# Kernel optimization log

Measured on AMD Instinct MI355X. Metric: run time of the kernel, lower is better.

Reference implementation:

```python
import jax, jax.numpy as jnp
import numpy as np

N, E, F, H, D, O = 100000, 1600000, 128, 128, 64, 1


def setup_inputs() -> dict:
    key = jax.random.key(0)
    ks = jax.random.split(key, 10)
    s = lambda f: np.float32(1.0 / np.sqrt(f))
    return {
        "x": jax.random.normal(ks[0], (N, F), jnp.float32),
        "edge_index": jax.random.randint(ks[1], (2, E), 0, N),
        "W1": jax.random.normal(ks[2], (F, H), jnp.float32) * s(F),
        "b1": jnp.zeros((H,), jnp.float32),
        "Wh": jax.random.normal(ks[3], (H, H), jnp.float32) * s(H),
        "bh": jnp.zeros((H,), jnp.float32),
        "W2": jax.random.normal(ks[4], (H, D), jnp.float32) * s(H),
        "b2": jnp.zeros((D,), jnp.float32),
        "Wo": jax.random.normal(ks[5], (D, O), jnp.float32) * s(D),
        "bo": jnp.zeros((O,), jnp.float32),
    }


def _gcn_layer(h, W, b, src, dst, norm, n):
    # linear transform then normalized sparse aggregation (GCNConv)
    h = h @ W                                   # [n, out]
    msg = h[src] * norm[:, None]                # gather + scale, [E+n, out]
    return jax.ops.segment_sum(msg, dst, num_segments=n) + b


def reference(x, edge_index, W1, b1, Wh, bh, W2, b2, Wo, bo):
    n = x.shape[0]
    loop = jnp.arange(n, dtype=edge_index.dtype)
    src = jnp.concatenate([edge_index[0], loop])  # add self loops
    dst = jnp.concatenate([edge_index[1], loop])
    deg = jax.ops.segment_sum(jnp.ones_like(dst, dtype=x.dtype), dst, num_segments=n)
    dinv = jnp.where(deg > 0, jax.lax.rsqrt(deg), 0.0)
    norm = dinv[src] * dinv[dst]                  # sym-normalized edge weights

    h = jax.nn.relu(_gcn_layer(x, W1, b1, src, dst, norm, n))
    h = jax.nn.relu(_gcn_layer(h, Wh, bh, src, dst, norm, n))
    z = _gcn_layer(h, W2, b2, src, dst, norm, n)  # embedding (no relu after gcn2)
    return z @ Wo + bo                            # node_classification logits [n, 1]
```

## Files before the change

kernel.cpp:

```cpp
#include <hip/hip_runtime.h>
#include <hip/hip_fp16.h>


#define CHUNK 8192
#define ASTR 136

using f16x8 = __attribute__((ext_vector_type(8))) _Float16;
using f32x4 = __attribute__((ext_vector_type(4))) float;

__global__ __launch_bounds__(256) void histH(const int* __restrict__ dst, int* __restrict__ hist,
                                             int E, int NBKT, int NB) {
    __shared__ int bins[1024];
    int blk = blockIdx.x;
    for (int i = threadIdx.x; i < NBKT; i += 256) bins[i] = 0;
    __syncthreads();
    int beg = blk * CHUNK, end = min(E, beg + CHUNK);
    for (int e = beg + threadIdx.x; e < end; e += 256)
        atomicAdd(&bins[dst[e] >> 7], 1);
    __syncthreads();
    for (int i = threadIdx.x; i < NBKT; i += 256)
        hist[i * NB + blk] = bins[i];
}

__global__ __launch_bounds__(256) void scanA(int* __restrict__ hist, int* __restrict__ binsum,
                                             int NBKT, int NB) {
    int wave = (int)((blockIdx.x * (size_t)blockDim.x + threadIdx.x) >> 6);
    if (wave >= NBKT) return;
    int lane = threadIdx.x & 63;
    int* row = hist + (size_t)wave * NB;
    int running = 0;
    for (int b0 = 0; b0 < NB; b0 += 64) {
        int idx = b0 + lane;
        int v = (idx < NB) ? row[idx] : 0;
        int s = v;
#pragma unroll
        for (int off = 1; off < 64; off <<= 1) {
            int u = __shfl_up(s, off, 64);
            if (lane >= off) s += u;
        }
        if (idx < NB) row[idx] = running + s - v;
        running += __shfl(s, 63, 64);
    }
    if (lane == 0) binsum[wave] = running;
}

__global__ void scanK2(const int* __restrict__ binsum, int* __restrict__ binbase,
                       int NBKT, int E) {
    __shared__ int s[1024];
    int t = threadIdx.x;
    int v = (t < NBKT) ? binsum[t] : 0;
    s[t] = v;
    __syncthreads();
    for (int off = 1; off < 1024; off <<= 1) {
        int u = (t >= off) ? s[t - off] : 0;
        __syncthreads();
        s[t] += u;
        __syncthreads();
    }
    if (t < NBKT) binbase[t] = s[t] - v;
    if (t == 0) binbase[NBKT] = E;
}

__global__ __launch_bounds__(256) void scatterH(const int* __restrict__ src,
                                                const int* __restrict__ dst,
                                                const int* __restrict__ hist,
                                                const int* __restrict__ binbase,
                                                int* __restrict__ tmp,
                                                int E, int NBKT, int NB) {
    __shared__ int offs[1024];
    int blk = blockIdx.x;
    for (int i = threadIdx.x; i < NBKT; i += 256)
        offs[i] = hist[i * NB + blk] + binbase[i];
    __syncthreads();
    int beg = blk * CHUNK, end = min(E, beg + CHUNK);
    for (int e = beg + threadIdx.x; e < end; e += 256) {
        int d = dst[e];
        int pos = atomicAdd(&offs[d >> 7], 1);
        tmp[pos] = ((d & 127) << 17) | src[e];
    }
}

__global__ __launch_bounds__(256) void bucket_csr(const int* __restrict__ tmp,
                                                  const int* __restrict__ binbase,
                                                  int* __restrict__ rowptr,
                                                  int* __restrict__ srcidx,
                                                  float* __restrict__ dinv,
                                                  int n) {
    __shared__ int cnt[128], sc[128], cnt2[128];
    int b = blockIdx.x;
    int bstart = binbase[b], bend = binbase[b + 1];
    if (threadIdx.x < 128) cnt[threadIdx.x] = 0;
    __syncthreads();
    for (int e = bstart + threadIdx.x; e < bend; e += 256)
        atomicAdd(&cnt[tmp[e] >> 17], 1);
    __syncthreads();
    if (threadIdx.x < 128) sc[threadIdx.x] = cnt[threadIdx.x];
    __syncthreads();
    for (int off = 1; off < 128; off <<= 1) {
        int u = 0;
        if (threadIdx.x < 128 && threadIdx.x >= off) u = sc[threadIdx.x - off];
        __syncthreads();
        if (threadIdx.x < 128) sc[threadIdx.x] += u;
        __syncthreads();
    }
    if (threadIdx.x < 128) {
        int excl = sc[threadIdx.x] - cnt[threadIdx.x];
        cnt2[threadIdx.x] = excl;
        int id = b * 128 + threadIdx.x;
        if (id <= n) rowptr[id] = bstart + excl;
        if (id < n) dinv[id] = rsqrtf((float)cnt[threadIdx.x] + 1.0f);
    }
    __syncthreads();
    for (int e = bstart + threadIdx.x; e < bend; e += 256) {
        int p = tmp[e];
        int pos = bstart + atomicAdd(&cnt2[p >> 17], 1);
        srcidx[pos] = p & 0x1FFFF;
    }
}

__global__ __launch_bounds__(256) void prep_w(const float* __restrict__ W1,
                                              const float* __restrict__ Wh,
                                              const float* __restrict__ W2,
                                              const float* __restrict__ b2,
                                              const float* __restrict__ Wo,
                                              const float* __restrict__ bo,
                                              __half* __restrict__ Wt1,
                                              __half* __restrict__ WtH,
                                              float* __restrict__ w3,
                                              float* __restrict__ c3) {
    const float* W = blockIdx.x ? Wh : W1;
    __half* Wt = blockIdx.x ? WtH : Wt1;
    for (int i = threadIdx.x; i < 16384; i += 256) {
        int c = i >> 7, k = i & 127;
        Wt[c * 128 + k] = __float2half(W[k * 128 + c]);
    }
    if (blockIdx.x == 0 && threadIdx.x < 128) {
        int j = threadIdx.x;
        float s = 0.f;
        for (int d = 0; d < 64; ++d) s += W2[j * 64 + d] * Wo[d];
        w3[j] = s;
        if (j == 0) {
            float c = 0.f;
            for (int d = 0; d < 64; ++d) c += b2[d] * Wo[d];
            *c3 = c + bo[0];
        }
    }
}

template<typename AT>
__global__ __launch_bounds__(256) void gemm_mfma(const AT* __restrict__ A,
                                                 const __half* __restrict__ Wt,
                                                 const float* __restrict__ dinv,
                                                 __half* __restrict__ Ch, int n) {
    __shared__ _Float16 Al[64 * ASTR];
    __shared__ _Float16 Wl[128 * ASTR];
    const int tid = threadIdx.x;
    const int row0 = blockIdx.x * 64;

#pragma unroll
    for (int i = 0; i < 8; ++i) {
        int idx = tid + 256 * i;
        int c = idx >> 4, q = idx & 15;
        uint4 v = *(const uint4*)(Wt + c * 128 + q * 8);
        *(uint4*)(&Wl[c * ASTR + q * 8]) = v;
    }
#pragma unroll
    for (int i = 0; i < 4; ++i) {
        int idx = tid + 256 * i;
        int r = idx >> 4, q = idx & 15;
        int row = row0 + r;
        uint4 u;
        if constexpr (sizeof(AT) == 2) {
            u = (row < n) ? *(const uint4*)((const __half*)A + (size_t)row * 128 + q * 8)
                          : make_uint4(0u, 0u, 0u, 0u);
        } else {
            if (row < n) {
                const float* ap = (const float*)A + (size_t)row * 128 + q * 8;
                float4 v0 = *(const float4*)ap;
                float4 v1 = *(const float4*)(ap + 4);
                __half2 p0 = __floats2half2_rn(v0.x, v0.y);
                __half2 p1 = __floats2half2_rn(v0.z, v0.w);
                __half2 p2 = __floats2half2_rn(v1.x, v1.y);
                __half2 p3 = __floats2half2_rn(v1.z, v1.w);
                u.x = *(unsigned*)&p0; u.y = *(unsigned*)&p1;
                u.z = *(unsigned*)&p2; u.w = *(unsigned*)&p3;
            } else u = make_uint4(0u, 0u, 0u, 0u);
        }
        *(uint4*)(&Al[r * ASTR + q * 8]) = u;
    }
    __syncthreads();

    const int wave = tid >> 6, lane = tid & 63;
    const int wr = (wave >> 1) * 32;
    const int wc = (wave & 1) * 64;
    const int l = lane & 15, g = lane >> 4;

    f32x4 acc[2][4];
#pragma unroll
    for (int i = 0; i < 2; ++i)
#pragma unroll
        for (int j = 0; j < 4; ++j) acc[i][j] = (f32x4){0.f, 0.f, 0.f, 0.f};

#pragma unroll
    for (int kk = 0; kk < 128; kk += 32) {
        int ko = kk + g * 8;
        f16x8 a0 = *(const f16x8*)(&Al[(wr + l) * ASTR + ko]);
        f16x8 a1 = *(const f16x8*)(&Al[(wr + 16 + l) * ASTR + ko]);
        f16x8 b0 = *(const f16x8*)(&Wl[(wc + l) * ASTR + ko]);
        f16x8 b1 = *(const f16x8*)(&Wl[(wc + 16 + l) * ASTR + ko]);
        f16x8 b2 = *(const f16x8*)(&Wl[(wc + 32 + l) * ASTR + ko]);
        f16x8 b3 = *(const f16x8*)(&Wl[(wc + 48 + l) * ASTR + ko]);
        acc[0][0] = __builtin_amdgcn_mfma_f32_16x16x32_f16(a0, b0, acc[0][0], 0, 0, 0);
        acc[0][1] = __builtin_amdgcn_mfma_f32_16x16x32_f16(a0, b1, acc[0][1], 0, 0, 0);
        acc[0][2] = __builtin_amdgcn_mfma_f32_16x16x32_f16(a0, b2, acc[0][2], 0, 0, 0);
        acc[0][3] = __builtin_amdgcn_mfma_f32_16x16x32_f16(a0, b3, acc[0][3], 0, 0, 0);
        acc[1][0] = __builtin_amdgcn_mfma_f32_16x16x32_f16(a1, b0, acc[1][0], 0, 0, 0);
        acc[1][1] = __builtin_amdgcn_mfma_f32_16x16x32_f16(a1, b1, acc[1][1], 0, 0, 0);
        acc[1][2] = __builtin_amdgcn_mfma_f32_16x16x32_f16(a1, b2, acc[1][2], 0, 0, 0);
        acc[1][3] = __builtin_amdgcn_mfma_f32_16x16x32_f16(a1, b3, acc[1][3], 0, 0, 0);
    }

#pragma unroll
    for (int rt = 0; rt < 2; ++rt) {
#pragma unroll
        for (int j = 0; j < 4; ++j) {
            int row = row0 + wr + rt * 16 + g * 4 + j;
            if (row < n) {
                float di = dinv[row];
#pragma unroll
                for (int ct = 0; ct < 4; ++ct)
                    Ch[(size_t)row * 128 + wc + ct * 16 + l] =
                        __float2half(acc[rt][ct][j] * di);
            }
        }
    }
}

template<int MODE>
__global__ __launch_bounds__(256) void agg_csr(const int* __restrict__ rowptr,
                                               const int* __restrict__ srcidx,
                                               const float* __restrict__ dinv,
                                               const __half* __restrict__ Gh,
                                               const float* __restrict__ bias,
                                               const float* __restrict__ w3,
                                               void* __restrict__ outp, int n) {
    int wid = (int)((blockIdx.x * (size_t)blockDim.x + threadIdx.x) >> 6);
    if (wid >= n) return;
    int lane = threadIdx.x & 63;
    int q = lane >> 4;
    int l = lane & 15;
    int beg = rowptr[wid], end = rowptr[wid + 1];
    const int co = l * 8;

    float4 aLo = make_float4(0.f, 0.f, 0.f, 0.f);
    float4 aHi = make_float4(0.f, 0.f, 0.f, 0.f);

#define ACC16(u)                                                            \
    {                                                                       \
        float2 f0 = __half22float2(*(const __half2*)&(u).x);                \
        float2 f1 = __half22float2(*(const __half2*)&(u).y);                \
        float2 f2 = __half22float2(*(const __half2*)&(u).z);                \
        float2 f3 = __half22float2(*(const __half2*)&(u).w);                \
        aLo.x += f0.x; aLo.y += f0.y; aLo.z += f1.x; aLo.w += f1.y;         \
        aHi.x += f2.x; aHi.y += f2.y; aHi.z += f3.x; aHi.w += f3.y;         \
    }

    if (q == 0) {
        uint4 u = *(const uint4*)(Gh + (size_t)wid * 128 + co);
        ACC16(u);
    }

    int e = beg + q;
    for (; e + 4 < end; e += 8) {
        int s0 = srcidx[e], s1 = srcidx[e + 4];
        uint4 u0 = *(const uint4*)(Gh + (size_t)s0 * 128 + co);
        uint4 u1 = *(const uint4*)(Gh + (size_t)s1 * 128 + co);
        ACC16(u0);
        ACC16(u1);
    }
    for (; e < end; e += 4) {
        int s0 = srcidx[e];
        uint4 u0 = *(const uint4*)(Gh + (size_t)s0 * 128 + co);
        ACC16(u0);
    }
#undef ACC16

    aLo.x += __shfl_xor(aLo.x, 16, 64); aLo.y += __shfl_xor(aLo.y, 16, 64);
    aLo.z += __shfl_xor(aLo.z, 16, 64); aLo.w += __shfl_xor(aLo.w, 16, 64);
    aHi.x += __shfl_xor(aHi.x, 16, 64); aHi.y += __shfl_xor(aHi.y, 16, 64);
    aHi.z += __shfl_xor(aHi.z, 16, 64); aHi.w += __shfl_xor(aHi.w, 16, 64);
    aLo.x += __shfl_xor(aLo.x, 32, 64); aLo.y += __shfl_xor(aLo.y, 32, 64);
    aLo.z += __shfl_xor(aLo.z, 32, 64); aLo.w += __shfl_xor(aLo.w, 32, 64);
    aHi.x += __shfl_xor(aHi.x, 32, 64); aHi.y += __shfl_xor(aHi.y, 32, 64);
    aHi.z += __shfl_xor(aHi.z, 32, 64); aHi.w += __shfl_xor(aHi.w, 32, 64);

    float di = dinv[wid];
    float4 b0 = *(const float4*)(bias + co);
    float4 b1 = *(const float4*)(bias + co + 4);
    float o0 = fmaxf(di * aLo.x + b0.x, 0.f);
    float o1 = fmaxf(di * aLo.y + b0.y, 0.f);
    float o2 = fmaxf(di * aLo.z + b0.z, 0.f);
    float o3 = fmaxf(di * aLo.w + b0.w, 0.f);
    float o4 = fmaxf(di * aHi.x + b1.x, 0.f);
    float o5 = fmaxf(di * aHi.y + b1.y, 0.f);
    float o6 = fmaxf(di * aHi.z + b1.z, 0.f);
    float o7 = fmaxf(di * aHi.w + b1.w, 0.f);

    if constexpr (MODE == 0) {
        if (lane < 16) {
            __half2 p0 = __floats2half2_rn(o0, o1);
            __half2 p1 = __floats2half2_rn(o2, o3);
            __half2 p2 = __floats2half2_rn(o4, o5);
            __half2 p3 = __floats2half2_rn(o6, o7);
            uint4 u;
            u.x = *(unsigned*)&p0; u.y = *(unsigned*)&p1;
            u.z = *(unsigned*)&p2; u.w = *(unsigned*)&p3;
            *(uint4*)((__half*)outp + (size_t)wid * 128 + co) = u;
        }
    } else {
        float4 w0 = *(const float4*)(w3 + co);
        float4 w1 = *(const float4*)(w3 + co + 4);
        float v = o0 * w0.x + o1 * w0.y + o2 * w0.z + o3 * w0.w
                + o4 * w1.x + o5 * w1.y + o6 * w1.z + o7 * w1.w;
        v += __shfl_xor(v, 1, 64);
        v += __shfl_xor(v, 2, 64);
        v += __shfl_xor(v, 4, 64);
        v += __shfl_xor(v, 8, 64);
        if (lane == 0) ((float*)outp)[wid] = di * v;
    }
}

__global__ void agg_csr_scalar(const int* __restrict__ rowptr, const int* __restrict__ srcidx,
                               const float* __restrict__ dinv, const float* __restrict__ ys,
                               const float* __restrict__ c3, float* __restrict__ out, int n) {
    int i = blockIdx.x * blockDim.x + threadIdx.x;
    if (i >= n) return;
    int beg = rowptr[i], end = rowptr[i + 1];
    float acc = ys[i];
    int e = beg;
    for (; e + 3 < end; e += 4) {
        acc += ys[srcidx[e]] + ys[srcidx[e + 1]] + ys[srcidx[e + 2]] + ys[srcidx[e + 3]];
    }
    for (; e < end; ++e) acc += ys[srcidx[e]];
    out[i] = dinv[i] * acc + c3[0];
}

static inline size_t align4(size_t x) { return (x + 3) & ~(size_t)3; }

extern "C" void kernel_launch(void* const* d_in, const int* in_sizes, int n_in,
                              void* d_out, int out_size, void* d_ws, size_t ws_size,
                              hipStream_t stream) {
    const float* x  = (const float*)d_in[0];
    const int* ei   = (const int*)d_in[1];
    const float* W1 = (const float*)d_in[2];
    const float* b1 = (const float*)d_in[3];
    const float* Wh = (const float*)d_in[4];
    const float* bh = (const float*)d_in[5];
    const float* W2 = (const float*)d_in[6];
    const float* b2 = (const float*)d_in[7];
    const float* Wo = (const float*)d_in[8];
    const float* bo = (const float*)d_in[9];
    float* out = (float*)d_out;

    const int n = in_sizes[0] / 128;
    const int E = in_sizes[1] / 2;
    const int* src = ei;
    const int* dst = ei + E;

    const int NB = (E + CHUNK - 1) / CHUNK;
    const int NBKT = (n >> 7) + 1;

    size_t o = 0;
    int* rowptr = (int*)d_ws + o;        o = align4(o + n + 1);
    int* srcidx = (int*)d_ws + o;        o = align4(o + E);
    int* hist   = (int*)d_ws + o;        o = align4(o + (size_t)NBKT * NB);
    int* binsum = (int*)d_ws + o;        o = align4(o + NBKT);
    int* binbase= (int*)d_ws + o;        o = align4(o + NBKT + 1);
    float* dinv = (float*)d_ws + o;      o = align4(o + n);
    float* w3   = (float*)d_ws + o;      o = align4(o + 128);
    float* c3   = (float*)d_ws + o;      o = align4(o + 4);
    __half* Wt1 = (__half*)((int*)d_ws + o);     o = align4(o + 8192);
    __half* WtH = (__half*)((int*)d_ws + o);     o = align4(o + 8192);
    __half* bufA16 = (__half*)((int*)d_ws + o);  o = align4(o + (size_t)n * 64);
    __half* bufB16 = (__half*)((int*)d_ws + o);  o = align4(o + (size_t)n * 64);
    int* tmp = (int*)bufA16;
    float* ys = (float*)bufB16;

    const int B = (n + 255) / 256;

    histH<<<NB, 256, 0, stream>>>(dst, hist, E, NBKT, NB);
    scanA<<<(NBKT * 64 + 255) / 256, 256, 0, stream>>>(hist, binsum, NBKT, NB);
    scanK2<<<1, 1024, 0, stream>>>(binsum, binbase, NBKT, E);
    scatterH<<<NB, 256, 0, stream>>>(src, dst, hist, binbase, tmp, E, NBKT, NB);
    bucket_csr<<<NBKT, 256, 0, stream>>>(tmp, binbase, rowptr, srcidx, dinv, n);
    prep_w<<<2, 256, 0, stream>>>(W1, Wh, W2, b2, Wo, bo, Wt1, WtH, w3, c3);

    const int GG = (n + 63) / 64;
    const int GA = (int)(((size_t)n * 64 + 255) / 256);

    gemm_mfma<float><<<GG, 256, 0, stream>>>(x, Wt1, dinv, bufA16, n);
    agg_csr<0><<<GA, 256, 0, stream>>>(rowptr, srcidx, dinv, bufA16, b1, w3, bufB16, n);

    gemm_mfma<__half><<<GG, 256, 0, stream>>>(bufB16, WtH, dinv, bufA16, n);
    agg_csr<1><<<GA, 256, 0, stream>>>(rowptr, srcidx, dinv, bufA16, bh, w3, ys, n);

    agg_csr_scalar<<<B, 256, 0, stream>>>(rowptr, srcidx, dinv, ys, c3, out, n);
}
```

Before: 240.2 us.

## Store features in 16-column slices and aggregate per slice for cache locality

The GEMM output and the input to the second GEMM switch from row-major [n,128] to eight column slices of [n,16]. The aggregation is split across blocks by slice, with 32 lanes per node, so each block's gathers hit a 3.2 MB slice table that fits better in L2/MALL. The second aggregation writes per-slice partial dot products that a new reduce8 kernel sums. In exchange each gather is only 32 bytes, edge indices are reread eight times, and there is an extra kernel launch plus an ys8 buffer.

```diff
diff --git a/kernel.cpp b/kernel.cpp
--- a/kernel.cpp
+++ b/kernel.cpp
@@ -171,8 +171,9 @@
         int row = row0 + r;
         uint4 u;
         if constexpr (sizeof(AT) == 2) {
-            u = (row < n) ? *(const uint4*)((const __half*)A + (size_t)row * 128 + q * 8)
-                          : make_uint4(0u, 0u, 0u, 0u);
+            const __half* ap = (const __half*)A + (size_t)(q >> 1) * n * 16
+                               + (size_t)row * 16 + (q & 1) * 8;
+            u = (row < n) ? *(const uint4*)ap : make_uint4(0u, 0u, 0u, 0u);
         } else {
             if (row < n) {
                 const float* ap = (const float*)A + (size_t)row * 128 + q * 8;
@@ -228,34 +229,33 @@
             if (row < n) {
                 float di = dinv[row];
 #pragma unroll
-                for (int ct = 0; ct < 4; ++ct)
-                    Ch[(size_t)row * 128 + wc + ct * 16 + l] =
+                for (int ct = 0; ct < 4; ++ct) {
+                    int slice = (wc >> 4) + ct;
+                    Ch[(size_t)slice * n * 16 + (size_t)row * 16 + l] =
                         __float2half(acc[rt][ct][j] * di);
+                }
             }
         }
     }
 }
 
 template<int MODE>
-__global__ __launch_bounds__(256) void agg_csr(const int* __restrict__ rowptr,
-                                               const int* __restrict__ srcidx,
-                                               const float* __restrict__ dinv,
-                                               const __half* __restrict__ Gh,
-                                               const float* __restrict__ bias,
-                                               const float* __restrict__ w3,
-                                               void* __restrict__ outp, int n) {
-    int wid = (int)((blockIdx.x * (size_t)blockDim.x + threadIdx.x) >> 6);
-    if (wid >= n) return;
-    int lane = threadIdx.x & 63;
-    int q = lane >> 4;
-    int l = lane & 15;
-    int beg = rowptr[wid], end = rowptr[wid + 1];
-    const int co = l * 8;
-
-    float4 aLo = make_float4(0.f, 0.f, 0.f, 0.f);
-    float4 aHi = make_float4(0.f, 0.f, 0.f, 0.f);
-
-#define ACC16(u)                                                            \
+__global__ __launch_bounds__(256) void agg_slice(const int* __restrict__ rowptr,
+                                                 const int* __restrict__ srcidx,
+                                                 const float* __restrict__ dinv,
+                                                 const __half* __restrict__ Gs,
+                                                 const float* __restrict__ bias,
+                                                 const float* __restrict__ w3,
+                                                 void* __restrict__ outp, int n) {
+    const int fb = blockIdx.x & 7;
+    const int chunk = blockIdx.x >> 3;
+    const int hw = threadIdx.x >> 5;
+    const int l = threadIdx.x & 31;
+    const int pair = l >> 1;
+    const int sub = l & 1;
+    const __half* T = Gs + (size_t)fb * n * 16;
+
+#define ACC8(u)                                                             \
     {                                                                       \
         float2 f0 = __half22float2(*(const __half2*)&(u).x);                \
         float2 f1 = __half22float2(*(const __half2*)&(u).y);                \
@@ -265,69 +265,79 @@
         aHi.x += f2.x; aHi.y += f2.y; aHi.z += f3.x; aHi.w += f3.y;         \
     }
 
-    if (q == 0) {
-        uint4 u = *(const uint4*)(Gh + (size_t)wid * 128 + co);
-        ACC16(u);
-    }
-
-    int e = beg + q;
-    for (; e + 4 < end; e += 8) {
-        int s0 = srcidx[e], s1 = srcidx[e + 4];
-        uint4 u0 = *(const uint4*)(Gh + (size_t)s0 * 128 + co);
-        uint4 u1 = *(const uint4*)(Gh + (size_t)s1 * 128 + co);
-        ACC16(u0);
-        ACC16(u1);
-    }
-    for (; e < end; e += 4) {
-        int s0 = srcidx[e];
-        uint4 u0 = *(const uint4*)(Gh + (size_t)s0 * 128 + co);
-        ACC16(u0);
-    }
-#undef ACC16
-
-    aLo.x += __shfl_xor(aLo.x, 16, 64); aLo.y += __shfl_xor(aLo.y, 16, 64);
-    aLo.z += __shfl_xor(aLo.z, 16, 64); aLo.w += __shfl_xor(aLo.w, 16, 64);
-    aHi.x += __shfl_xor(aHi.x, 16, 64); aHi.y += __shfl_xor(aHi.y, 16, 64);
-    aHi.z += __shfl_xor(aHi.z, 16, 64); aHi.w += __shfl_xor(aHi.w, 16, 64);
-    aLo.x += __shfl_xor(aLo.x, 32, 64); aLo.y += __shfl_xor(aLo.y, 32, 64);
-    aLo.z += __shfl_xor(aLo.z, 32, 64); aLo.w += __shfl_xor(aLo.w, 32, 64);
-    aHi.x += __shfl_xor(aHi.x, 32, 64); aHi.y += __shfl_xor(aHi.y, 32, 64);
-    aHi.z += __shfl_xor(aHi.z, 32, 64); aHi.w += __shfl_xor(aHi.w, 32, 64);
-
-    float di = dinv[wid];
-    float4 b0 = *(const float4*)(bias + co);
-    float4 b1 = *(const float4*)(bias + co + 4);
-    float o0 = fmaxf(di * aLo.x + b0.x, 0.f);
-    float o1 = fmaxf(di * aLo.y + b0.y, 0.f);
-    float o2 = fmaxf(di * aLo.z + b0.z, 0.f);
-    float o3 = fmaxf(di * aLo.w + b0.w, 0.f);
-    float o4 = fmaxf(di * aHi.x + b1.x, 0.f);
-    float o5 = fmaxf(di * aHi.y + b1.y, 0.f);
-    float o6 = fmaxf(di * aHi.z + b1.z, 0.f);
-    float o7 = fmaxf(di * aHi.w + b1.w, 0.f);
-
-    if constexpr (MODE == 0) {
-        if (lane < 16) {
-            __half2 p0 = __floats2half2_rn(o0, o1);
-            __half2 p1 = __floats2half2_rn(o2, o3);
-            __half2 p2 = __floats2half2_rn(o4, o5);
-            __half2 p3 = __floats2half2_rn(o6, o7);
-            uint4 u;
-            u.x = *(unsigned*)&p0; u.y = *(unsigned*)&p1;
-            u.z = *(unsigned*)&p2; u.w = *(unsigned*)&p3;
-            *(uint4*)((__half*)outp + (size_t)wid * 128 + co) = u;
-        }
-    } else {
-        float4 w0 = *(const float4*)(w3 + co);
-        float4 w1 = *(const float4*)(w3 + co + 4);
-        float v = o0 * w0.x + o1 * w0.y + o2 * w0.z + o3 * w0.w
-                + o4 * w1.x + o5 * w1.y + o6 * w1.z + o7 * w1.w;
-        v += __shfl_xor(v, 1, 64);
-        v += __shfl_xor(v, 2, 64);
-        v += __shfl_xor(v, 4, 64);
-        v += __shfl_xor(v, 8, 64);
-        if (lane == 0) ((float*)outp)[wid] = di * v;
-    }
+#pragma unroll
+    for (int nd = 0; nd < 4; ++nd) {
+        int node = chunk * 32 + hw * 4 + nd;
+        if (node >= n) return;
+        int beg = rowptr[node], end = rowptr[node + 1];
+
+        float4 aLo = make_float4(0.f, 0.f, 0.f, 0.f);
+        float4 aHi = make_float4(0.f, 0.f, 0.f, 0.f);
+
+        if (pair == 0) {
+            uint4 u = *(const uint4*)(T + (size_t)node * 16 + sub * 8);
+            ACC8(u);
+        }
+        for (int e = beg + pair; e < end; e += 16) {
+            int s = srcidx[e];
+            uint4 u = *(const uint4*)(T + (size_t)s * 16 + sub * 8);
+            ACC8(u);
+        }
+
+#pragma unroll
+        for (int m = 2; m <= 16; m <<= 1) {
+            aLo.x += __shfl_xor(aLo.x, m, 64); aLo.y += __shfl_xor(aLo.y, m, 64);
+            aLo.z += __shfl_xor(aLo.z, m, 64); aLo.w += __shfl_xor(aLo.w, m, 64);
+            aHi.x += __shfl_xor(aHi.x, m, 64); aHi.y += __shfl_xor(aHi.y, m, 64);
+            aHi.z += __shfl_xor(aHi.z, m, 64); aHi.w += __shfl_xor(aHi.w, m, 64);
+        }
+
+        float di = dinv[node];
+        const float* bp = bias + fb * 16 + sub * 8;
+        float4 b0 = *(const float4*)bp;
+        float4 b1 = *(const float4*)(bp + 4);
+        float o0 = fmaxf(di * aLo.x + b0.x, 0.f);
+        float o1 = fmaxf(di * aLo.y + b0.y, 0.f);
+        float o2 = fmaxf(di * aLo.z + b0.z, 0.f);
+        float o3 = fmaxf(di * aLo.w + b0.w, 0.f);
+        float o4 = fmaxf(di * aHi.x + b1.x, 0.f);
+        float o5 = fmaxf(di * aHi.y + b1.y, 0.f);
+        float o6 = fmaxf(di * aHi.z + b1.z, 0.f);
+        float o7 = fmaxf(di * aHi.w + b1.w, 0.f);
+
+        if constexpr (MODE == 0) {
+            if (pair == 0) {
+                __half2 p0 = __floats2half2_rn(o0, o1);
+                __half2 p1 = __floats2half2_rn(o2, o3);
+                __half2 p2 = __floats2half2_rn(o4, o5);
+                __half2 p3 = __floats2half2_rn(o6, o7);
+                uint4 u;
+                u.x = *(unsigned*)&p0; u.y = *(unsigned*)&p1;
+                u.z = *(unsigned*)&p2; u.w = *(unsigned*)&p3;
+                *(uint4*)((__half*)outp + (size_t)fb * n * 16
+                          + (size_t)node * 16 + sub * 8) = u;
+            }
+        } else {
+            const float* wp = w3 + fb * 16 + sub * 8;
+            float4 w0 = *(const float4*)wp;
+            float4 w1 = *(const float4*)(wp + 4);
+            float v = o0 * w0.x + o1 * w0.y + o2 * w0.z + o3 * w0.w
+                    + o4 * w1.x + o5 * w1.y + o6 * w1.z + o7 * w1.w;
+            v += __shfl_xor(v, 1, 64);
+            if (l == 0) ((float*)outp)[(size_t)fb * n + node] = v;
+        }
+    }
+#undef ACC8
+}
+
+__global__ void reduce8(const float* __restrict__ ys8, const float* __restrict__ dinv,
+                        float* __restrict__ ys, int n) {
+    int i = blockIdx.x * blockDim.x + threadIdx.x;
+    if (i >= n) return;
+    float s = 0.f;
+#pragma unroll
+    for (int f = 0; f < 8; ++f) s += ys8[(size_t)f * n + i];
+    ys[i] = dinv[i] * s;
 }
 
 __global__ void agg_csr_scalar(const int* __restrict__ rowptr, const int* __restrict__ srcidx,
@@ -383,8 +393,9 @@
     __half* WtH = (__half*)((int*)d_ws + o);     o = align4(o + 8192);
     __half* bufA16 = (__half*)((int*)d_ws + o);  o = align4(o + (size_t)n * 64);
     __half* bufB16 = (__half*)((int*)d_ws + o);  o = align4(o + (size_t)n * 64);
+    float* ys8 = (float*)((int*)d_ws + o);       o = align4(o + (size_t)n * 8);
     int* tmp = (int*)bufA16;
-    float* ys = (float*)bufB16;
+    float* ys = (float*)bufA16;
 
     const int B = (n + 255) / 256;
 
@@ -396,13 +407,14 @@
     prep_w<<<2, 256, 0, stream>>>(W1, Wh, W2, b2, Wo, bo, Wt1, WtH, w3, c3);
 
     const int GG = (n + 63) / 64;
-    const int GA = (int)(((size_t)n * 64 + 255) / 256);
+    const int GA = ((n + 31) / 32) * 8;
 
     gemm_mfma<float><<<GG, 256, 0, stream>>>(x, Wt1, dinv, bufA16, n);
-    agg_csr<0><<<GA, 256, 0, stream>>>(rowptr, srcidx, dinv, bufA16, b1, w3, bufB16, n);
+    agg_slice<0><<<GA, 256, 0, stream>>>(rowptr, srcidx, dinv, bufA16, b1, w3, bufB16, n);
 
     gemm_mfma<__half><<<GG, 256, 0, stream>>>(bufB16, WtH, dinv, bufA16, n);
-    agg_csr<1><<<GA, 256, 0, stream>>>(rowptr, srcidx, dinv, bufA16, bh, w3, ys, n);
-
+    agg_slice<1><<<GA, 256, 0, stream>>>(rowptr, srcidx, dinv, bufA16, bh, w3, ys8, n);
+
+    reduce8<<<B, 256, 0, stream>>>(ys8, dinv, ys, n);
     agg_csr_scalar<<<B, 256, 0, stream>>>(rowptr, srcidx, dinv, ys, c3, out, n);
 }
```

Measured after the change: 403.5 us. +68.0%, slower.
